# Kernel tuning notes

Hardware: AMD Instinct MI355X
Metric: run time of the kernel (lower is better)

Reference implementation:

```python
import jax, jax.numpy as jnp
import numpy as np

SCALE_DIM = 128  # d_k


def setup_inputs() -> dict:
    key = jax.random.key(0)
    k1, k2, k3, k4 = jax.random.split(key, 4)
    BH, T, D = 32, 2048, 128
    query = jax.random.normal(k1, (BH, T, D), dtype=jnp.float32)
    key_t = jax.random.normal(k2, (BH, T, D), dtype=jnp.float32)
    value = jax.random.normal(k3, (BH, T, D), dtype=jnp.float32)
    key_padding_mask = jax.random.randint(k4, (BH, T), 0, 2).astype(jnp.bool_)
    return {"query": query, "key": key_t, "value": value,
            "key_padding_mask": key_padding_mask}


def reference(query, key, value, key_padding_mask):
    # attn_logits: (BH, T_q, T_k)
    d_k = key.shape[-1]
    logits = jnp.einsum('bqd,bkd->bqk', query, key) / jnp.sqrt(
        jnp.asarray(d_k, dtype=query.dtype))
    # key_padding_mask (BH, T_k): True means masked out
    logits = jnp.where(key_padding_mask[:, None, :], -jnp.inf, logits)
    # softmax in float32 (as the torch code does), dropout p=0.0 is identity
    attention = jax.nn.softmax(logits.astype(jnp.float32), axis=-1).astype(query.dtype)
    out = jnp.einsum('bqk,bkd->bqd', attention, value)
    return out
```

## Files before the change

kernel.cpp:

```cpp
#include <hip/hip_runtime.h>
#include <hip/hip_fp16.h>


#define BHN  32
#define TSEQ 2048
#define DDIM 128
#define QB   256
#define WQ   32
#define KB   64
#define NKT  (TSEQ / KB)

typedef __attribute__((ext_vector_type(4))) float    f32x4;
typedef __attribute__((ext_vector_type(8))) _Float16 f16x8;
typedef __attribute__((ext_vector_type(4))) _Float16 f16x4;

__device__ __forceinline__ unsigned kaddr(int row, int d) {
    return ((unsigned)(row * 256 + d * 2)) ^ ((unsigned)(row & 7) << 4);
}
__device__ __forceinline__ unsigned vaddr(int d, int kvp) {
    return ((unsigned)(d * 128 + kvp * 2)) ^ (((unsigned)((d ^ (d >> 3)) & 7)) << 4);
}

__global__ __launch_bounds__(512, 2)
void attn_fwd(const float* __restrict__ Qg, const float* __restrict__ Kg,
              const float* __restrict__ Vg, const unsigned char* __restrict__ Mg,
              float* __restrict__ Og)
{
    __shared__ __align__(16) unsigned short Kh[2][KB * DDIM];
    __shared__ __align__(16) unsigned short Vt[2][DDIM * KB];
    __shared__ float biasLds[2][KB];
    __shared__ int mflag;

    const int tid  = threadIdx.x;
    const int lane = tid & 63;
    const int wave = tid >> 6;
    const int q16  = lane & 15;
    const int hi   = lane >> 4;

    const int bh    = blockIdx.x;
    const int qbase = blockIdx.y * QB + wave * WQ;

    const float scale = 0.088388347648318447f;

    const float* Qp = Qg + ((size_t)bh * TSEQ + qbase) * DDIM;
    const float* Kp = Kg + (size_t)bh * TSEQ * DDIM;
    const float* Vp = Vg + (size_t)bh * TSEQ * DDIM;

    if (tid == 0) mflag = 0;
    __syncthreads();
    {
        int f = 0;
#pragma unroll
        for (int j = 0; j < 4; ++j) {
            const int idx = tid * 4 + j;
            if ((idx & 3) != 0 && Mg[idx] != 0) f = 1;
        }
        if (f) atomicOr(&mflag, 1);
    }
    __syncthreads();
    const int isByte = mflag;

    f16x8 qf[2][4];
#pragma unroll
    for (int qt = 0; qt < 2; ++qt) {
        const float* qrow = Qp + (size_t)(qt * 16 + q16) * DDIM;
#pragma unroll
        for (int c = 0; c < 4; ++c) {
            const int d0 = 32 * c + 8 * hi;
            f32x4 a = *reinterpret_cast<const f32x4*>(qrow + d0);
            f32x4 b = *reinterpret_cast<const f32x4*>(qrow + d0 + 4);
            f16x8 f;
#pragma unroll
            for (int i = 0; i < 8; ++i)
                f[i] = (_Float16)((i < 4 ? a[i] : b[i - 4]) * scale);
            qf[qt][c] = f;
        }
    }

    f32x4 o[2][8];
#pragma unroll
    for (int qt = 0; qt < 2; ++qt)
#pragma unroll
        for (int db = 0; db < 8; ++db)
            o[qt][db] = (f32x4){0.f, 0.f, 0.f, 0.f};
    float mrun[2] = {-1e30f, -1e30f};
    float lrun[2] = {0.f, 0.f};

    const int sd   = (tid & 31) * 4;
    const int qrw  = (((tid >> 5) & 1) << 2) | ((tid >> 6) & 3) | (((tid >> 8) & 1) << 3);
    const int rb   = qrw * 4;
    const int kvpb = (((qrw >> 2) & 1) << 2) | ((qrw & 3) << 3) | (((qrw >> 3) & 1) << 5);

    f32x4 kreg[4], vreg[4];
    int mreg = 0;

#define LOAD_TILE(kv0)                                                              \
    {                                                                               \
        _Pragma("unroll")                                                           \
        for (int r = 0; r < 4; ++r) {                                               \
            kreg[r] = *reinterpret_cast<const f32x4*>(Kp + (size_t)((kv0) + rb + r) * DDIM + sd); \
            vreg[r] = *reinterpret_cast<const f32x4*>(Vp + (size_t)((kv0) + rb + r) * DDIM + sd); \
        }                                                                           \
        if (tid < KB) {                                                             \
            const size_t mi = (size_t)bh * TSEQ + (kv0) + tid;                      \
            mreg = isByte ? (int)Mg[mi] : ((const int*)Mg)[mi];                     \
        }                                                                           \
    }

#define STORE_TILE(b)                                                               \
    {                                                                               \
        if (tid < KB) biasLds[b][tid] = mreg ? -1e30f : 0.0f;                       \
        char* khb = reinterpret_cast<char*>(&Kh[b][0]);                             \
        char* vtb = reinterpret_cast<char*>(&Vt[b][0]);                             \
        _Pragma("unroll")                                                           \
        for (int r = 0; r < 4; ++r) {                                               \
            f16x4 k4;                                                               \
            k4[0] = (_Float16)kreg[r][0]; k4[1] = (_Float16)kreg[r][1];             \
            k4[2] = (_Float16)kreg[r][2]; k4[3] = (_Float16)kreg[r][3];             \
            *reinterpret_cast<f16x4*>(khb + kaddr(rb + r, sd)) = k4;                \
        }                                                                           \
        _Pragma("unroll")                                                           \
        for (int j = 0; j < 4; ++j) {                                               \
            f16x4 v4;                                                               \
            v4[0] = (_Float16)vreg[0][j]; v4[1] = (_Float16)vreg[1][j];             \
            v4[2] = (_Float16)vreg[2][j]; v4[3] = (_Float16)vreg[3][j];             \
            *reinterpret_cast<f16x4*>(vtb + vaddr(sd + j, kvpb)) = v4;              \
        }                                                                           \
    }

    LOAD_TILE(0);
    STORE_TILE(0);
    __syncthreads();

    for (int kt = 0; kt < NKT; ++kt) {
        const int cur = kt & 1;
        if (kt + 1 < NKT) LOAD_TILE((kt + 1) * KB);

        const char* khb = reinterpret_cast<const char*>(&Kh[cur][0]);
        const char* vtb = reinterpret_cast<const char*>(&Vt[cur][0]);

        f32x4 st[2][4];
#pragma unroll
        for (int t = 0; t < 4; ++t) {
            f32x4 binit;
#pragma unroll
            for (int r = 0; r < 4; ++r) binit[r] = biasLds[cur][16 * t + 4 * hi + r];
            st[0][t] = binit;
            st[1][t] = binit;
        }
        __builtin_amdgcn_s_setprio(1);
#pragma unroll
        for (int t = 0; t < 4; ++t) {
#pragma unroll
            for (int c = 0; c < 4; ++c) {
                const unsigned ka = kaddr(16 * t + q16, 32 * c + 8 * hi);
                f16x8 kf = *reinterpret_cast<const f16x8*>(khb + ka);
                st[0][t] = __builtin_amdgcn_mfma_f32_16x16x32_f16(kf, qf[0][c], st[0][t], 0, 0, 0);
                st[1][t] = __builtin_amdgcn_mfma_f32_16x16x32_f16(kf, qf[1][c], st[1][t], 0, 0, 0);
            }
        }
        __builtin_amdgcn_s_setprio(0);

        f16x8 pf[2][2];
        float resc[2];
#pragma unroll
        for (int qt = 0; qt < 2; ++qt) {
            float mx = st[qt][0][0];
#pragma unroll
            for (int t = 0; t < 4; ++t)
#pragma unroll
                for (int r = 0; r < 4; ++r)
                    mx = fmaxf(mx, st[qt][t][r]);
            mx = fmaxf(mx, __shfl_xor(mx, 16));
            mx = fmaxf(mx, __shfl_xor(mx, 32));
            const float mnew = fmaxf(mrun[qt], mx);
            const float rs   = __expf(mrun[qt] - mnew);
            mrun[qt] = mnew;
            resc[qt] = rs;
            float ps = 0.f;
            float pv[4][4];
#pragma unroll
            for (int t = 0; t < 4; ++t)
#pragma unroll
                for (int r = 0; r < 4; ++r) {
                    const float e = __expf(st[qt][t][r] - mnew);
                    pv[t][r] = e;
                    ps += e;
                }
            ps += __shfl_xor(ps, 16);
            ps += __shfl_xor(ps, 32);
            lrun[qt] = lrun[qt] * rs + ps;
#pragma unroll
            for (int h = 0; h < 2; ++h) {
                f16x8 f;
#pragma unroll
                for (int r = 0; r < 4; ++r) {
                    f[r]     = (_Float16)pv[2 * h][r];
                    f[r + 4] = (_Float16)pv[2 * h + 1][r];
                }
                pf[qt][h] = f;
            }
        }
#pragma unroll
        for (int qt = 0; qt < 2; ++qt)
#pragma unroll
            for (int r = 0; r < 4; ++r) {
                const int src = (lane & 48) | (4 * hi + r);
                const float rr = __shfl(resc[qt], src);
#pragma unroll
                for (int db = 0; db < 8; ++db)
                    o[qt][db][r] *= rr;
            }

        __builtin_amdgcn_s_setprio(1);
#pragma unroll
        for (int db = 0; db < 8; ++db) {
            const int d = db * 16 + q16;
            f16x8 vfrag[2];
#pragma unroll
            for (int h = 0; h < 2; ++h)
                vfrag[h] = *reinterpret_cast<const f16x8*>(vtb + vaddr(d, 32 * h + 8 * hi));
            o[0][db] = __builtin_amdgcn_mfma_f32_16x16x32_f16(pf[0][0], vfrag[0], o[0][db], 0, 0, 0);
            o[0][db] = __builtin_amdgcn_mfma_f32_16x16x32_f16(pf[0][1], vfrag[1], o[0][db], 0, 0, 0);
            o[1][db] = __builtin_amdgcn_mfma_f32_16x16x32_f16(pf[1][0], vfrag[0], o[1][db], 0, 0, 0);
            o[1][db] = __builtin_amdgcn_mfma_f32_16x16x32_f16(pf[1][1], vfrag[1], o[1][db], 0, 0, 0);
        }
        __builtin_amdgcn_s_setprio(0);

        if (kt + 1 < NKT) STORE_TILE(cur ^ 1);
        __syncthreads();
    }

    float* Op = Og + ((size_t)bh * TSEQ + qbase) * DDIM;
#pragma unroll
    for (int qt = 0; qt < 2; ++qt)
#pragma unroll
        for (int r = 0; r < 4; ++r) {
            const int src = (lane & 48) | (4 * hi + r);
            const float inv = 1.0f / __shfl(lrun[qt], src);
            const int qrow = qt * 16 + 4 * hi + r;
#pragma unroll
            for (int db = 0; db < 8; ++db)
                Op[(size_t)qrow * DDIM + db * 16 + q16] = o[qt][db][r] * inv;
        }
}

extern "C" void kernel_launch(void* const* d_in, const int* in_sizes, int n_in,
                              void* d_out, int out_size, void* d_ws, size_t ws_size,
                              hipStream_t stream) {
    const float* q = (const float*)d_in[0];
    const float* k = (const float*)d_in[1];
    const float* v = (const float*)d_in[2];
    const unsigned char* m = (const unsigned char*)d_in[3];
    float* out = (float*)d_out;
    dim3 grid(BHN, TSEQ / QB);
    dim3 block(512);
    attn_fwd<<<grid, block, 0, stream>>>(q, k, v, m, out);
}
```

Before: 209.0 us.

## Halve queries per wave, fold log2e into the Q scale, and rescale lazily

The query block shrinks from 256 to 128 rows, so each wave owns one 16-row query tile instead of two. This doubles the grid, which should fill more CUs and lower register pressure per wave, at the cost of reloading K/V tiles twice as often. The softmax now uses exp2f with log2(e) folded into the Q scaling. The running-max rescale of the accumulators is skipped unless some row's max rises by more than 8, in log2 units, above the stored max. That cuts per-tile exp and multiply work but lets unnormalised exponentials reach up to 256 before conversion to fp16.

```diff
diff --git a/kernel.cpp b/kernel.cpp
--- a/kernel.cpp
+++ b/kernel.cpp
@@ -5,8 +5,7 @@
 #define BHN  32
 #define TSEQ 2048
 #define DDIM 128
-#define QB   256
-#define WQ   32
+#define QB   128
 #define KB   64
 #define NKT  (TSEQ / KB)
 
@@ -38,9 +37,9 @@
     const int hi   = lane >> 4;
 
     const int bh    = blockIdx.x;
-    const int qbase = blockIdx.y * QB + wave * WQ;
-
-    const float scale = 0.088388347648318447f;
+    const int qbase = blockIdx.y * QB + wave * 16;
+
+    const float scale = 0.088388347648318447f * 1.4426950408889634f;
 
     const float* Qp = Qg + ((size_t)bh * TSEQ + qbase) * DDIM;
     const float* Kp = Kg + (size_t)bh * TSEQ * DDIM;
@@ -60,10 +59,9 @@
     __syncthreads();
     const int isByte = mflag;
 
-    f16x8 qf[2][4];
-#pragma unroll
-    for (int qt = 0; qt < 2; ++qt) {
-        const float* qrow = Qp + (size_t)(qt * 16 + q16) * DDIM;
+    f16x8 qf[4];
+    {
+        const float* qrow = Qp + (size_t)q16 * DDIM;
 #pragma unroll
         for (int c = 0; c < 4; ++c) {
             const int d0 = 32 * c + 8 * hi;
@@ -73,18 +71,16 @@
 #pragma unroll
             for (int i = 0; i < 8; ++i)
                 f[i] = (_Float16)((i < 4 ? a[i] : b[i - 4]) * scale);
-            qf[qt][c] = f;
-        }
-    }
-
-    f32x4 o[2][8];
-#pragma unroll
-    for (int qt = 0; qt < 2; ++qt)
-#pragma unroll
-        for (int db = 0; db < 8; ++db)
-            o[qt][db] = (f32x4){0.f, 0.f, 0.f, 0.f};
-    float mrun[2] = {-1e30f, -1e30f};
-    float lrun[2] = {0.f, 0.f};
+            qf[c] = f;
+        }
+    }
+
+    f32x4 o[8];
+#pragma unroll
+    for (int db = 0; db < 8; ++db)
+        o[db] = (f32x4){0.f, 0.f, 0.f, 0.f};
+    float mrun = -1e30f;
+    float lrun = 0.f;
 
     const int sd   = (tid & 31) * 4;
     const int qrw  = (((tid >> 5) & 1) << 2) | ((tid >> 6) & 3) | (((tid >> 8) & 1) << 3);
@@ -139,14 +135,13 @@
         const char* khb = reinterpret_cast<const char*>(&Kh[cur][0]);
         const char* vtb = reinterpret_cast<const char*>(&Vt[cur][0]);
 
-        f32x4 st[2][4];
+        f32x4 st[4];
 #pragma unroll
         for (int t = 0; t < 4; ++t) {
             f32x4 binit;
 #pragma unroll
             for (int r = 0; r < 4; ++r) binit[r] = biasLds[cur][16 * t + 4 * hi + r];
-            st[0][t] = binit;
-            st[1][t] = binit;
+            st[t] = binit;
         }
         __builtin_amdgcn_s_setprio(1);
 #pragma unroll
@@ -155,75 +150,68 @@
             for (int c = 0; c < 4; ++c) {
                 const unsigned ka = kaddr(16 * t + q16, 32 * c + 8 * hi);
                 f16x8 kf = *reinterpret_cast<const f16x8*>(khb + ka);
-                st[0][t] = __builtin_amdgcn_mfma_f32_16x16x32_f16(kf, qf[0][c], st[0][t], 0, 0, 0);
-                st[1][t] = __builtin_amdgcn_mfma_f32_16x16x32_f16(kf, qf[1][c], st[1][t], 0, 0, 0);
+                st[t] = __builtin_amdgcn_mfma_f32_16x16x32_f16(kf, qf[c], st[t], 0, 0, 0);
             }
         }
         __builtin_amdgcn_s_setprio(0);
 
-        f16x8 pf[2][2];
-        float resc[2];
-#pragma unroll
-        for (int qt = 0; qt < 2; ++qt) {
-            float mx = st[qt][0][0];
-#pragma unroll
-            for (int t = 0; t < 4; ++t)
-#pragma unroll
-                for (int r = 0; r < 4; ++r)
-                    mx = fmaxf(mx, st[qt][t][r]);
-            mx = fmaxf(mx, __shfl_xor(mx, 16));
-            mx = fmaxf(mx, __shfl_xor(mx, 32));
-            const float mnew = fmaxf(mrun[qt], mx);
-            const float rs   = __expf(mrun[qt] - mnew);
-            mrun[qt] = mnew;
-            resc[qt] = rs;
-            float ps = 0.f;
-            float pv[4][4];
-#pragma unroll
-            for (int t = 0; t < 4; ++t)
-#pragma unroll
-                for (int r = 0; r < 4; ++r) {
-                    const float e = __expf(st[qt][t][r] - mnew);
-                    pv[t][r] = e;
-                    ps += e;
-                }
-            ps += __shfl_xor(ps, 16);
-            ps += __shfl_xor(ps, 32);
-            lrun[qt] = lrun[qt] * rs + ps;
-#pragma unroll
-            for (int h = 0; h < 2; ++h) {
-                f16x8 f;
-#pragma unroll
-                for (int r = 0; r < 4; ++r) {
-                    f[r]     = (_Float16)pv[2 * h][r];
-                    f[r + 4] = (_Float16)pv[2 * h + 1][r];
-                }
-                pf[qt][h] = f;
-            }
-        }
-#pragma unroll
-        for (int qt = 0; qt < 2; ++qt)
+        float mx = st[0][0];
+#pragma unroll
+        for (int t = 0; t < 4; ++t)
+#pragma unroll
+            for (int r = 0; r < 4; ++r)
+                mx = fmaxf(mx, st[t][r]);
+        mx = fmaxf(mx, __shfl_xor(mx, 16));
+        mx = fmaxf(mx, __shfl_xor(mx, 32));
+
+        if (!__all(mx <= mrun + 8.0f)) {
+            const float mnew = fmaxf(mrun, mx);
+            const float rs   = exp2f(mrun - mnew);
+            mrun = mnew;
+            lrun *= rs;
 #pragma unroll
             for (int r = 0; r < 4; ++r) {
                 const int src = (lane & 48) | (4 * hi + r);
-                const float rr = __shfl(resc[qt], src);
+                const float rr = __shfl(rs, src);
 #pragma unroll
                 for (int db = 0; db < 8; ++db)
-                    o[qt][db][r] *= rr;
-            }
+                    o[db][r] *= rr;
+            }
+        }
+
+        float ps = 0.f;
+        float pv[4][4];
+#pragma unroll
+        for (int t = 0; t < 4; ++t)
+#pragma unroll
+            for (int r = 0; r < 4; ++r) {
+                const float e = exp2f(st[t][r] - mrun);
+                pv[t][r] = e;
+                ps += e;
+            }
+        ps += __shfl_xor(ps, 16);
+        ps += __shfl_xor(ps, 32);
+        lrun += ps;
+        f16x8 pf[2];
+#pragma unroll
+        for (int h = 0; h < 2; ++h) {
+            f16x8 f;
+#pragma unroll
+            for (int r = 0; r < 4; ++r) {
+                f[r]     = (_Float16)pv[2 * h][r];
+                f[r + 4] = (_Float16)pv[2 * h + 1][r];
+            }
+            pf[h] = f;
+        }
 
         __builtin_amdgcn_s_setprio(1);
 #pragma unroll
         for (int db = 0; db < 8; ++db) {
             const int d = db * 16 + q16;
-            f16x8 vfrag[2];
-#pragma unroll
-            for (int h = 0; h < 2; ++h)
-                vfrag[h] = *reinterpret_cast<const f16x8*>(vtb + vaddr(d, 32 * h + 8 * hi));
-            o[0][db] = __builtin_amdgcn_mfma_f32_16x16x32_f16(pf[0][0], vfrag[0], o[0][db], 0, 0, 0);
-            o[0][db] = __builtin_amdgcn_mfma_f32_16x16x32_f16(pf[0][1], vfrag[1], o[0][db], 0, 0, 0);
-            o[1][db] = __builtin_amdgcn_mfma_f32_16x16x32_f16(pf[1][0], vfrag[0], o[1][db], 0, 0, 0);
-            o[1][db] = __builtin_amdgcn_mfma_f32_16x16x32_f16(pf[1][1], vfrag[1], o[1][db], 0, 0, 0);
+            f16x8 v0 = *reinterpret_cast<const f16x8*>(vtb + vaddr(d, 8 * hi));
+            f16x8 v1 = *reinterpret_cast<const f16x8*>(vtb + vaddr(d, 32 + 8 * hi));
+            o[db] = __builtin_amdgcn_mfma_f32_16x16x32_f16(pf[0], v0, o[db], 0, 0, 0);
+            o[db] = __builtin_amdgcn_mfma_f32_16x16x32_f16(pf[1], v1, o[db], 0, 0, 0);
         }
         __builtin_amdgcn_s_setprio(0);
 
@@ -233,16 +221,14 @@
 
     float* Op = Og + ((size_t)bh * TSEQ + qbase) * DDIM;
 #pragma unroll
-    for (int qt = 0; qt < 2; ++qt)
-#pragma unroll
-        for (int r = 0; r < 4; ++r) {
-            const int src = (lane & 48) | (4 * hi + r);
-            const float inv = 1.0f / __shfl(lrun[qt], src);
-            const int qrow = qt * 16 + 4 * hi + r;
-#pragma unroll
-            for (int db = 0; db < 8; ++db)
-                Op[(size_t)qrow * DDIM + db * 16 + q16] = o[qt][db][r] * inv;
-        }
+    for (int r = 0; r < 4; ++r) {
+        const int src = (lane & 48) | (4 * hi + r);
+        const float inv = 1.0f / __shfl(lrun, src);
+        const int qrow = 4 * hi + r;
+#pragma unroll
+        for (int db = 0; db < 8; ++db)
+            Op[(size_t)qrow * DDIM + db * 16 + q16] = o[db][r] * inv;
+    }
 }
 
 extern "C" void kernel_launch(void* const* d_in, const int* in_sizes, int n_in,
```

Result: slower. 246.7 us (+18.0%).

## Use exp2 with log2e-folded scale and lazily rescale the online-softmax accumulator

Applied to the files above, without the earlier changes.

Folds log2(e) into the Q scale so the softmax exponentials use exp2f in place of __expf. The running max and the output rescale now run only when some lane's new tile max exceeds the stored max by more than 8 (log2 units), so most tiles skip the shuffle-and-multiply over all 64 accumulator registers. The risk is that un-rescaled exponentials can reach 2^8, which cuts fp16 headroom for P and adds a warp-uniform branch. The V-fragment load is also rewritten into two named loads, which is cosmetic.

```diff
diff --git a/kernel.cpp b/kernel.cpp
--- a/kernel.cpp
+++ b/kernel.cpp
@@ -6,7 +6,6 @@
 #define TSEQ 2048
 #define DDIM 128
 #define QB   256
-#define WQ   32
 #define KB   64
 #define NKT  (TSEQ / KB)
 
@@ -38,9 +37,9 @@
     const int hi   = lane >> 4;
 
     const int bh    = blockIdx.x;
-    const int qbase = blockIdx.y * QB + wave * WQ;
-
-    const float scale = 0.088388347648318447f;
+    const int qbase = blockIdx.y * QB + wave * 32;
+
+    const float scale = 0.088388347648318447f * 1.4426950408889634f;
 
     const float* Qp = Qg + ((size_t)bh * TSEQ + qbase) * DDIM;
     const float* Kp = Kg + (size_t)bh * TSEQ * DDIM;
@@ -162,7 +161,6 @@
         __builtin_amdgcn_s_setprio(0);
 
         f16x8 pf[2][2];
-        float resc[2];
 #pragma unroll
         for (int qt = 0; qt < 2; ++qt) {
             float mx = st[qt][0][0];
@@ -173,23 +171,35 @@
                     mx = fmaxf(mx, st[qt][t][r]);
             mx = fmaxf(mx, __shfl_xor(mx, 16));
             mx = fmaxf(mx, __shfl_xor(mx, 32));
-            const float mnew = fmaxf(mrun[qt], mx);
-            const float rs   = __expf(mrun[qt] - mnew);
-            mrun[qt] = mnew;
-            resc[qt] = rs;
+
+            if (!__all(mx <= mrun[qt] + 8.0f)) {
+                const float mnew = fmaxf(mrun[qt], mx);
+                const float rs   = exp2f(mrun[qt] - mnew);
+                mrun[qt] = mnew;
+                lrun[qt] *= rs;
+#pragma unroll
+                for (int r = 0; r < 4; ++r) {
+                    const int src = (lane & 48) | (4 * hi + r);
+                    const float rr = __shfl(rs, src);
+#pragma unroll
+                    for (int db = 0; db < 8; ++db)
+                        o[qt][db][r] *= rr;
+                }
+            }
+
             float ps = 0.f;
             float pv[4][4];
 #pragma unroll
             for (int t = 0; t < 4; ++t)
 #pragma unroll
                 for (int r = 0; r < 4; ++r) {
-                    const float e = __expf(st[qt][t][r] - mnew);
+                    const float e = exp2f(st[qt][t][r] - mrun[qt]);
                     pv[t][r] = e;
                     ps += e;
                 }
             ps += __shfl_xor(ps, 16);
             ps += __shfl_xor(ps, 32);
-            lrun[qt] = lrun[qt] * rs + ps;
+            lrun[qt] += ps;
 #pragma unroll
             for (int h = 0; h < 2; ++h) {
                 f16x8 f;
@@ -201,29 +211,17 @@
                 pf[qt][h] = f;
             }
         }
-#pragma unroll
-        for (int qt = 0; qt < 2; ++qt)
-#pragma unroll
-            for (int r = 0; r < 4; ++r) {
-                const int src = (lane & 48) | (4 * hi + r);
-                const float rr = __shfl(resc[qt], src);
-#pragma unroll
-                for (int db = 0; db < 8; ++db)
-                    o[qt][db][r] *= rr;
-            }
 
         __builtin_amdgcn_s_setprio(1);
 #pragma unroll
         for (int db = 0; db < 8; ++db) {
             const int d = db * 16 + q16;
-            f16x8 vfrag[2];
-#pragma unroll
-            for (int h = 0; h < 2; ++h)
-                vfrag[h] = *reinterpret_cast<const f16x8*>(vtb + vaddr(d, 32 * h + 8 * hi));
-            o[0][db] = __builtin_amdgcn_mfma_f32_16x16x32_f16(pf[0][0], vfrag[0], o[0][db], 0, 0, 0);
-            o[0][db] = __builtin_amdgcn_mfma_f32_16x16x32_f16(pf[0][1], vfrag[1], o[0][db], 0, 0, 0);
-            o[1][db] = __builtin_amdgcn_mfma_f32_16x16x32_f16(pf[1][0], vfrag[0], o[1][db], 0, 0, 0);
-            o[1][db] = __builtin_amdgcn_mfma_f32_16x16x32_f16(pf[1][1], vfrag[1], o[1][db], 0, 0, 0);
+            f16x8 v0 = *reinterpret_cast<const f16x8*>(vtb + vaddr(d, 8 * hi));
+            f16x8 v1 = *reinterpret_cast<const f16x8*>(vtb + vaddr(d, 32 + 8 * hi));
+            o[0][db] = __builtin_amdgcn_mfma_f32_16x16x32_f16(pf[0][0], v0, o[0][db], 0, 0, 0);
+            o[0][db] = __builtin_amdgcn_mfma_f32_16x16x32_f16(pf[0][1], v1, o[0][db], 0, 0, 0);
+            o[1][db] = __builtin_amdgcn_mfma_f32_16x16x32_f16(pf[1][0], v0, o[1][db], 0, 0, 0);
+            o[1][db] = __builtin_amdgcn_mfma_f32_16x16x32_f16(pf[1][1], v1, o[1][db], 0, 0, 0);
         }
         __builtin_amdgcn_s_setprio(0);
 
```

Measured after the change: 212.9 us. No clear change (+1.9%).
